# Optimization experiments

Measured on AMD Instinct MI355X. Metric: run time of the kernel, lower is better.

Reference implementation:

```python
import jax, jax.numpy as jnp
import numpy as np

N = 65536       # n_nodes
E = 1048576     # n_edges (avg degree 16)
D = 64          # in_features == out_features
GAMMA = 1.0


def setup_inputs() -> dict:
    key = jax.random.key(0)
    k_x, k_x0, k_ev, k_w, k_er, k_ec = jax.random.split(key, 6)
    x = jax.random.normal(k_x, (N, D), dtype=jnp.float32)
    x_0 = jax.random.normal(k_x0, (N, D), dtype=jnp.float32)
    edge_val = jax.random.uniform(k_ev, (E,), dtype=jnp.float32)
    # xavier_uniform for [D, D]: bound = sqrt(6 / (D + D))
    bound = np.sqrt(6.0 / (D + D)).astype(np.float32)
    weight = jax.random.uniform(k_w, (D, D), dtype=jnp.float32, minval=-bound, maxval=bound)
    bias = jnp.zeros((D,), dtype=jnp.float32)
    edge_row = jax.random.randint(k_er, (E,), 0, N, dtype=jnp.int32)
    edge_col = jax.random.randint(k_ec, (E,), 0, N, dtype=jnp.int32)
    return {"x": x, "x_0": x_0, "edge_val": edge_val, "weight": weight,
            "bias": bias, "edge_row": edge_row, "edge_col": edge_col}


def reference(x, x_0, edge_val, weight, bias, edge_row, edge_col):
    d = weight.shape[0]
    eye = jnp.eye(d, dtype=weight.dtype)
    s = weight - weight.T                      # skew-symmetric part
    m_left = eye - s
    m_right = eye + s
    # ortho_weight = solve(I + s, (I - s)^T)^T  (Cayley transform as written)
    ortho_weight = jnp.linalg.solve(m_right, m_left.T).T
    support = x @ ortho_weight                 # [N, D] dense GEMM
    # sparse adjacency spmm via COO gather + segment-sum
    gathered = edge_val[:, None] * support[edge_col]          # [E, D]
    agg = jax.ops.segment_sum(gathered, edge_row, num_segments=x.shape[0])  # [N, D]
    out = agg * GAMMA + x_0 + bias
    return out
```

## Files before the change

### kernel.cpp

```cpp
#include <hip/hip_runtime.h>
#include <math.h>


#define DFEAT 64
#define RPB   64
#define NPART_MAX 1024
#define EPB   4096
#define CURS  16
#define C_ROW 32
#define SPMM_T 512


__global__ void zero_ints_kernel(int* __restrict__ p, int n) {
    int i = blockIdx.x * blockDim.x + threadIdx.x;
    if (i < n) p[i] = 0;
}

__global__ void x_to_bf16_kernel(const float* __restrict__ x,
                                 unsigned short* __restrict__ x16, int n4) {
    int i = blockIdx.x * blockDim.x + threadIdx.x;
    if (i >= n4) return;
    float4 v = ((const float4*)x)[i];
    ushort4 o;
    unsigned u;
    u = __float_as_uint(v.x); o.x = (unsigned short)((u + 0x7FFFu + ((u >> 16) & 1u)) >> 16);
    u = __float_as_uint(v.y); o.y = (unsigned short)((u + 0x7FFFu + ((u >> 16) & 1u)) >> 16);
    u = __float_as_uint(v.z); o.z = (unsigned short)((u + 0x7FFFu + ((u >> 16) & 1u)) >> 16);
    u = __float_as_uint(v.w); o.w = (unsigned short)((u + 0x7FFFu + ((u >> 16) & 1u)) >> 16);
    ((ushort4*)x16)[i] = o;
}

__global__ __launch_bounds__(1024) void partition_build_kernel(
        const int* __restrict__ edge_row,
        const int* __restrict__ edge_col,
        const float* __restrict__ edge_val,
        int* __restrict__ scursor,
        int2* __restrict__ slists,
        int* __restrict__ ov_cursor,
        int2* __restrict__ ov_list,
        int E, int NP, int pcap) {
    __shared__ int cnt[NPART_MAX];
    __shared__ int off[NPART_MAX];
    int t = threadIdx.x;
    int base = blockIdx.x * EPB;
    int end = base + EPB; if (end > E) end = E;

    for (int i = t; i < NP; i += 1024) cnt[i] = 0;
    __syncthreads();
    for (int e = base + t; e < end; e += 1024)
        atomicAdd(&cnt[edge_row[e] >> 6], 1);
    __syncthreads();
    for (int p = t; p < NP; p += 1024) {
        int c = cnt[p];
        off[p] = (c > 0) ? atomicAdd(&scursor[p * CURS], c) : 0;
    }
    __syncthreads();
    for (int e = base + t; e < end; e += 1024) {
        int r = edge_row[e];
        int p = r >> 6;
        int2 ent;
        ent.x = (int)(((unsigned)r << 16) | (unsigned)edge_col[e]);
        ent.y = __float_as_int(edge_val[e]);
        int pos = atomicAdd(&off[p], 1);
        if (pos < pcap) {
            slists[(size_t)p * pcap + pos] = ent;
        } else {
            int op = atomicAdd(ov_cursor, 1);
            ov_list[op] = ent;
        }
    }
}

__global__ __launch_bounds__(SPMM_T) void spmm_fused_kernel(
        const unsigned short* __restrict__ x16,
        const float* __restrict__ x0,
        const float* __restrict__ bias,
        const int* __restrict__ scursor,
        const int2* __restrict__ slists,
        int* __restrict__ ov_cursor,
        int2* __restrict__ ov_list,
        float* __restrict__ out, int pcap) {
    __shared__ int2 bkt[RPB * C_ROW];
    __shared__ int  cur[RPB];
    int p = blockIdx.x;
    int t = threadIdx.x;

    if (t < RPB) cur[t] = 0;
    for (int i = t; i < RPB * C_ROW; i += SPMM_T) bkt[i] = make_int2(0, 0);
    __syncthreads();

    int cnt = scursor[p * CURS];
    if (cnt > pcap) cnt = pcap;
    const int2* list = slists + (size_t)p * pcap;
    for (int i = t; i < cnt; i += SPMM_T) {
        int2 ent = list[i];
        int row = (int)(((unsigned)ent.x >> 16) & (RPB - 1));
        int pos = atomicAdd(&cur[row], 1);
        if (pos < C_ROW) {
            bkt[row * C_ROW + pos] = ent;
        } else {
            int op = atomicAdd(ov_cursor, 1);
            ov_list[op] = ent;
        }
    }
    __syncthreads();

    int wave = t >> 6, lane = t & 63;
    float bl = bias[lane];
    for (int rr = wave; rr < RPB; rr += (SPMM_T / 64)) {
        int cr = cur[rr]; if (cr > C_ROW) cr = C_ROW;
        int cr8 = (cr + 7) & ~7;
        const int2* rb = &bkt[rr * C_ROW];
        float acc = 0.f;
        for (int j0 = 0; j0 < cr8; j0 += 8) {
            float xv[8], vv[8];
            #pragma unroll
            for (int k = 0; k < 8; k++) {
                int2 e = rb[j0 + k];
                vv[k] = __int_as_float(e.y);
                unsigned short hv =
                    x16[(size_t)((unsigned)e.x & 0xFFFFu) * DFEAT + lane];
                xv[k] = __uint_as_float((unsigned)hv << 16);
            }
            #pragma unroll
            for (int k = 0; k < 8; k++)
                acc += vv[k] * xv[k];
        }
        size_t go = (size_t)(p * RPB + rr) * DFEAT + lane;
        out[go] = acc + x0[go] + bl;
    }
}

__global__ void ov_drain_packed_kernel(const float* __restrict__ x,
                                       const int* __restrict__ ov_cursor,
                                       const int2* __restrict__ ov_list,
                                       float* __restrict__ out, int cap) {
    int n = ov_cursor[0];
    if (n > cap) n = cap;
    int wid = (blockIdx.x * blockDim.x + threadIdx.x) >> 6;
    int lane = threadIdx.x & 63;
    int nw = (gridDim.x * blockDim.x) >> 6;
    for (int k = wid; k < n; k += nw) {
        int2 p = ov_list[k];
        unsigned ux = (unsigned)p.x;
        int r = (int)(ux >> 16);
        int c = (int)(ux & 0xFFFFu);
        float v = __int_as_float(p.y);
        atomicAdd(&out[(size_t)r * DFEAT + lane],
                  v * x[(size_t)c * DFEAT + lane]);
    }
}


__global__ void bucket_scatter_kernel(const int* __restrict__ edge_row,
                                      const int* __restrict__ edge_col,
                                      const float* __restrict__ edge_val,
                                      int* __restrict__ cursor,
                                      int2* __restrict__ bucket,
                                      int* __restrict__ ov_cursor,
                                      int* __restrict__ ov_list,
                                      int E, int C) {
    int e = blockIdx.x * blockDim.x + threadIdx.x;
    if (e >= E) return;
    int r = edge_row[e];
    int pos = atomicAdd(&cursor[r], 1);
    if (pos < C) {
        int2 ent;
        ent.x = edge_col[e];
        ent.y = __float_as_int(edge_val[e]);
        bucket[(size_t)r * C + pos] = ent;
    } else {
        int op = atomicAdd(ov_cursor, 1);
        ov_list[op] = e;
    }
}

__global__ __launch_bounds__(256) void spmm_kernel(
        const float* __restrict__ x,
        const float* __restrict__ x0,
        const float* __restrict__ bias,
        const int* __restrict__ counts,
        const int2* __restrict__ bucket,
        float* __restrict__ out, int n, int C) {
    int wid = (blockIdx.x * blockDim.x + threadIdx.x) >> 6;
    int lane = threadIdx.x & 63;
    if (wid >= n) return;
    int cnt = counts[wid];
    if (cnt > C) cnt = C;
    const int2* bk = bucket + (size_t)wid * C;
    float acc = 0.f;
    for (int s0 = 0; s0 < cnt; s0 += 64) {
        int m = cnt - s0; if (m > 64) m = 64;
        int c = 0; float v = 0.f;
        if (lane < m) {
            int2 p = bk[s0 + lane];
            c = p.x;
            v = __int_as_float(p.y);
        }
        for (int j0 = 0; j0 < m; j0 += 8) {
            float xv[8], vv[8];
            #pragma unroll
            for (int k = 0; k < 8; k++) {
                int cj = __builtin_amdgcn_readlane(c, j0 + k);
                int vb = __builtin_amdgcn_readlane(__float_as_int(v), j0 + k);
                vv[k] = __int_as_float(vb);
                xv[k] = x[(size_t)cj * DFEAT + lane];
            }
            #pragma unroll
            for (int k = 0; k < 8; k++)
                acc += vv[k] * xv[k];
        }
    }
    out[(size_t)wid * DFEAT + lane] =
        acc + x0[(size_t)wid * DFEAT + lane] + bias[lane];
}

__global__ void ov_drain_id_kernel(const int* __restrict__ edge_row,
                                   const int* __restrict__ edge_col,
                                   const float* __restrict__ edge_val,
                                   const float* __restrict__ x,
                                   const int* __restrict__ ov_cursor,
                                   const int* __restrict__ ov_list,
                                   float* __restrict__ out, int E) {
    int n = ov_cursor[0];
    if (n > E) n = E;
    int wid = (blockIdx.x * blockDim.x + threadIdx.x) >> 6;
    int lane = threadIdx.x & 63;
    int nw = (gridDim.x * blockDim.x) >> 6;
    for (int k = wid; k < n; k += nw) {
        int e = ov_list[k];
        int r = edge_row[e], c = edge_col[e];
        float v = edge_val[e];
        atomicAdd(&out[(size_t)r * DFEAT + lane],
                  v * x[(size_t)c * DFEAT + lane]);
    }
}


__global__ void init_out_kernel(const float* __restrict__ x0,
                                const float* __restrict__ bias,
                                float* __restrict__ out, int n4) {
    int i = blockIdx.x * blockDim.x + threadIdx.x;
    if (i < n4) {
        float4 v = ((const float4*)x0)[i];
        int d = (i * 4) & (DFEAT - 1);
        v.x += bias[d + 0]; v.y += bias[d + 1];
        v.z += bias[d + 2]; v.w += bias[d + 3];
        ((float4*)out)[i] = v;
    }
}

__global__ void edge_scatter_kernel(const float* __restrict__ x,
                                    const float* __restrict__ edge_val,
                                    const int* __restrict__ edge_row,
                                    const int* __restrict__ edge_col,
                                    float* __restrict__ out, int E) {
    int tid = blockIdx.x * blockDim.x + threadIdx.x;
    int wave = tid >> 6, lane = tid & 63;
    int nwaves = (gridDim.x * blockDim.x) >> 6;
    for (int e = wave; e < E; e += nwaves) {
        int row = edge_row[e];
        int col = edge_col[e];
        float val = edge_val[e];
        atomicAdd(&out[row * DFEAT + lane], val * x[col * DFEAT + lane]);
    }
}

extern "C" void kernel_launch(void* const* d_in, const int* in_sizes, int n_in,
                              void* d_out, int out_size, void* d_ws, size_t ws_size,
                              hipStream_t stream) {
    const float* x    = (const float*)d_in[0];
    const float* x0   = (const float*)d_in[1];
    const float* ev   = (const float*)d_in[2];
    const float* bias = (const float*)d_in[4];
    const int*   er   = (const int*)d_in[5];
    const int*   ec   = (const int*)d_in[6];
    float* out = (float*)d_out;

    int E = in_sizes[2];
    int N = out_size / DFEAT;

    auto align256 = [](size_t b) { return (b + 255) & ~size_t(255); };

    if (N <= 65536 && N % RPB == 0 && E > 0) {
        int NP = N / RPB;
        double avg = (double)E / (double)NP;
        int pcap = (int)(avg + 6.0 * sqrt(avg > 1.0 ? avg : 1.0) + 64.0);

        size_t scur_b = align256((size_t)NP * CURS * 4);
        size_t ovc_b  = 256;
        size_t x16_b  = align256((size_t)N * DFEAT * 2);
        size_t ov_b   = align256((size_t)E * 8);
        size_t sl_b   = align256((size_t)NP * (size_t)pcap * 8);
        size_t total  = scur_b + ovc_b + x16_b + ov_b + sl_b;

        if (total <= ws_size) {
            char* ws = (char*)d_ws;
            int*            scursor = (int*)ws;
            int*            ovc     = (int*)(ws + scur_b);
            unsigned short* x16     = (unsigned short*)(ws + scur_b + ovc_b);
            int2*           ov_list = (int2*)(ws + scur_b + ovc_b + x16_b);
            int2*           slists  = (int2*)(ws + scur_b + ovc_b + x16_b + ov_b);

            int nzero = (int)((scur_b + ovc_b) / 4);
            zero_ints_kernel<<<(nzero + 255) / 256, 256, 0, stream>>>(scursor, nzero);
            int n4 = N * DFEAT / 4;
            x_to_bf16_kernel<<<(n4 + 255) / 256, 256, 0, stream>>>(x, x16, n4);
            int nblk = (E + EPB - 1) / EPB;
            partition_build_kernel<<<nblk, 1024, 0, stream>>>(
                er, ec, ev, scursor, slists, ovc, ov_list, E, NP, pcap);
            spmm_fused_kernel<<<NP, SPMM_T, 0, stream>>>(
                x16, x0, bias, scursor, slists, ovc, ov_list, out, pcap);
            ov_drain_packed_kernel<<<64, 256, 0, stream>>>(
                x, ovc, ov_list, out, E);
            return;
        }
    }

    {
        size_t cur_b = align256((size_t)N * 4);
        size_t ovc_b = 256;
        size_t ov_b  = align256((size_t)E * 4);
        size_t fixed = cur_b + ovc_b + ov_b;
        int C = 0;
        if (ws_size > fixed) {
            long long cmax = (long long)((ws_size - fixed) / ((size_t)N * 8));
            for (int cand : {64, 48, 40, 32, 28, 24})
                if (cmax >= cand) { C = cand; break; }
        }
        if (C >= 24) {
            char* ws = (char*)d_ws;
            int*  cursor  = (int*)ws;
            int*  ovc     = (int*)(ws + cur_b);
            int*  ov_list = (int*)(ws + cur_b + ovc_b);
            int2* bucket  = (int2*)(ws + fixed);

            int nzero = (int)((cur_b + ovc_b) / 4);
            zero_ints_kernel<<<(nzero + 255) / 256, 256, 0, stream>>>(cursor, nzero);
            bucket_scatter_kernel<<<(E + 255) / 256, 256, 0, stream>>>(
                er, ec, ev, cursor, bucket, ovc, ov_list, E, C);
            int blocks = (N * 64 + 255) / 256;
            spmm_kernel<<<blocks, 256, 0, stream>>>(
                x, x0, bias, cursor, bucket, out, N, C);
            ov_drain_id_kernel<<<64, 256, 0, stream>>>(
                er, ec, ev, x, ovc, ov_list, out, E);
            return;
        }
    }

    int n4 = out_size / 4;
    init_out_kernel<<<(n4 + 255) / 256, 256, 0, stream>>>(x0, bias, out, n4);
    edge_scatter_kernel<<<8192, 256, 0, stream>>>(x, ev, er, ec, out, E);
}
```

Baseline: 148.1 us.

## Replace global partition cursors with per-block private slot lists and fuse bf16 conversion

The partition build now gives each of 256 builder blocks a private fixed-capacity slot region per partition, so the global atomic cursor reservation and the per-block counting pass go away. Per-block counts are written to a table that the SpMM kernel reads to skip empty slots. The x-to-bf16 conversion is merged into the build kernel as extra blocks, which removes one launch and the large zeroing kernel. In exchange the SpMM kernel now scans 256×CAP slots per partition, many of them empty, and the sparse slot buffer is larger, which adds strided reads.

```diff
diff --git a/kernel.cpp b/kernel.cpp
--- a/kernel.cpp
+++ b/kernel.cpp
@@ -5,8 +5,7 @@
 #define DFEAT 64
 #define RPB   64
 #define NPART_MAX 1024
-#define EPB   4096
-#define CURS  16
+#define BBLK  256
 #define C_ROW 32
 #define SPMM_T 512
 
@@ -16,58 +15,62 @@
     if (i < n) p[i] = 0;
 }
 
-__global__ void x_to_bf16_kernel(const float* __restrict__ x,
-                                 unsigned short* __restrict__ x16, int n4) {
-    int i = blockIdx.x * blockDim.x + threadIdx.x;
-    if (i >= n4) return;
-    float4 v = ((const float4*)x)[i];
-    ushort4 o;
-    unsigned u;
-    u = __float_as_uint(v.x); o.x = (unsigned short)((u + 0x7FFFu + ((u >> 16) & 1u)) >> 16);
-    u = __float_as_uint(v.y); o.y = (unsigned short)((u + 0x7FFFu + ((u >> 16) & 1u)) >> 16);
-    u = __float_as_uint(v.z); o.z = (unsigned short)((u + 0x7FFFu + ((u >> 16) & 1u)) >> 16);
-    u = __float_as_uint(v.w); o.w = (unsigned short)((u + 0x7FFFu + ((u >> 16) & 1u)) >> 16);
-    ((ushort4*)x16)[i] = o;
-}
-
-__global__ __launch_bounds__(1024) void partition_build_kernel(
+__global__ __launch_bounds__(1024) void build_conv_kernel(
         const int* __restrict__ edge_row,
         const int* __restrict__ edge_col,
         const float* __restrict__ edge_val,
-        int* __restrict__ scursor,
+        const float* __restrict__ x,
+        unsigned short* __restrict__ x16,
+        int* __restrict__ cnt_blk,
         int2* __restrict__ slists,
         int* __restrict__ ov_cursor,
         int2* __restrict__ ov_list,
-        int E, int NP, int pcap) {
-    __shared__ int cnt[NPART_MAX];
-    __shared__ int off[NPART_MAX];
+        int E, int NP, int cap_shift, int n4) {
+    __shared__ int cur[NPART_MAX];
     int t = threadIdx.x;
-    int base = blockIdx.x * EPB;
-    int end = base + EPB; if (end > E) end = E;
-
-    for (int i = t; i < NP; i += 1024) cnt[i] = 0;
+
+    if (blockIdx.x >= BBLK) {
+        int i = (blockIdx.x - BBLK) * 1024 + t;
+        if (i < n4) {
+            float4 v = ((const float4*)x)[i];
+            ushort4 o;
+            unsigned u;
+            u = __float_as_uint(v.x); o.x = (unsigned short)((u + 0x7FFFu + ((u >> 16) & 1u)) >> 16);
+            u = __float_as_uint(v.y); o.y = (unsigned short)((u + 0x7FFFu + ((u >> 16) & 1u)) >> 16);
+            u = __float_as_uint(v.z); o.z = (unsigned short)((u + 0x7FFFu + ((u >> 16) & 1u)) >> 16);
+            u = __float_as_uint(v.w); o.w = (unsigned short)((u + 0x7FFFu + ((u >> 16) & 1u)) >> 16);
+            ((ushort4*)x16)[i] = o;
+        }
+        return;
+    }
+
+    int b = blockIdx.x;
+    int epb = (E + BBLK - 1) / BBLK;
+    int base = b * epb;
+    int end = base + epb; if (end > E) end = E;
+    int CAP = 1 << cap_shift;
+
+    for (int i = t; i < NP; i += 1024) cur[i] = 0;
     __syncthreads();
-    for (int e = base + t; e < end; e += 1024)
-        atomicAdd(&cnt[edge_row[e] >> 6], 1);
-    __syncthreads();
-    for (int p = t; p < NP; p += 1024) {
-        int c = cnt[p];
-        off[p] = (c > 0) ? atomicAdd(&scursor[p * CURS], c) : 0;
-    }
-    __syncthreads();
+
     for (int e = base + t; e < end; e += 1024) {
         int r = edge_row[e];
         int p = r >> 6;
         int2 ent;
         ent.x = (int)(((unsigned)r << 16) | (unsigned)edge_col[e]);
         ent.y = __float_as_int(edge_val[e]);
-        int pos = atomicAdd(&off[p], 1);
-        if (pos < pcap) {
-            slists[(size_t)p * pcap + pos] = ent;
+        int pos = atomicAdd(&cur[p], 1);
+        if (pos < CAP) {
+            slists[((((size_t)p << 8) | (size_t)b) << cap_shift) + pos] = ent;
         } else {
             int op = atomicAdd(ov_cursor, 1);
             ov_list[op] = ent;
         }
+    }
+    __syncthreads();
+    for (int p = t; p < NP; p += 1024) {
+        int c = cur[p];
+        cnt_blk[(size_t)b * NP + p] = (c > CAP) ? CAP : c;
     }
 }
 
@@ -75,32 +78,39 @@
         const unsigned short* __restrict__ x16,
         const float* __restrict__ x0,
         const float* __restrict__ bias,
-        const int* __restrict__ scursor,
+        const int* __restrict__ cnt_blk,
         const int2* __restrict__ slists,
         int* __restrict__ ov_cursor,
         int2* __restrict__ ov_list,
-        float* __restrict__ out, int pcap) {
+        float* __restrict__ out, int NP, int cap_shift) {
     __shared__ int2 bkt[RPB * C_ROW];
     __shared__ int  cur[RPB];
+    __shared__ int  ccnt[BBLK];
     int p = blockIdx.x;
     int t = threadIdx.x;
 
     if (t < RPB) cur[t] = 0;
+    for (int i = t; i < BBLK; i += SPMM_T)
+        ccnt[i] = cnt_blk[(size_t)i * NP + p];
     for (int i = t; i < RPB * C_ROW; i += SPMM_T) bkt[i] = make_int2(0, 0);
     __syncthreads();
 
-    int cnt = scursor[p * CURS];
-    if (cnt > pcap) cnt = pcap;
-    const int2* list = slists + (size_t)p * pcap;
-    for (int i = t; i < cnt; i += SPMM_T) {
-        int2 ent = list[i];
-        int row = (int)(((unsigned)ent.x >> 16) & (RPB - 1));
-        int pos = atomicAdd(&cur[row], 1);
-        if (pos < C_ROW) {
-            bkt[row * C_ROW + pos] = ent;
-        } else {
-            int op = atomicAdd(ov_cursor, 1);
-            ov_list[op] = ent;
+    int CAP = 1 << cap_shift;
+    int slots = BBLK << cap_shift;
+    const int2* list = slists + (((size_t)p << 8) << cap_shift);
+    for (int i = t; i < slots; i += SPMM_T) {
+        int b = i >> cap_shift;
+        int j = i & (CAP - 1);
+        if (j < ccnt[b]) {
+            int2 ent = list[i];
+            int row = (int)(((unsigned)ent.x >> 16) & (RPB - 1));
+            int pos = atomicAdd(&cur[row], 1);
+            if (pos < C_ROW) {
+                bkt[row * C_ROW + pos] = ent;
+            } else {
+                int op = atomicAdd(ov_cursor, 1);
+                ov_list[op] = ent;
+            }
         }
     }
     __syncthreads();
@@ -284,33 +294,35 @@
 
     if (N <= 65536 && N % RPB == 0 && E > 0) {
         int NP = N / RPB;
-        double avg = (double)E / (double)NP;
-        int pcap = (int)(avg + 6.0 * sqrt(avg > 1.0 ? avg : 1.0) + 64.0);
-
-        size_t scur_b = align256((size_t)NP * CURS * 4);
+        double lam = (double)E / ((double)NP * (double)BBLK);
+        double want = lam + 6.0 * sqrt(lam > 1.0 ? lam : 1.0);
+        int cap_shift = 4;
+        while ((double)(1 << cap_shift) < want && cap_shift < 10) cap_shift++;
+        size_t CAP = (size_t)1 << cap_shift;
+
         size_t ovc_b  = 256;
         size_t x16_b  = align256((size_t)N * DFEAT * 2);
         size_t ov_b   = align256((size_t)E * 8);
-        size_t sl_b   = align256((size_t)NP * (size_t)pcap * 8);
-        size_t total  = scur_b + ovc_b + x16_b + ov_b + sl_b;
+        size_t cnt_b  = align256((size_t)BBLK * (size_t)NP * 4);
+        size_t sl_b   = align256((size_t)NP * BBLK * CAP * 8);
+        size_t total  = ovc_b + x16_b + ov_b + cnt_b + sl_b;
 
         if (total <= ws_size) {
             char* ws = (char*)d_ws;
-            int*            scursor = (int*)ws;
-            int*            ovc     = (int*)(ws + scur_b);
-            unsigned short* x16     = (unsigned short*)(ws + scur_b + ovc_b);
-            int2*           ov_list = (int2*)(ws + scur_b + ovc_b + x16_b);
-            int2*           slists  = (int2*)(ws + scur_b + ovc_b + x16_b + ov_b);
-
-            int nzero = (int)((scur_b + ovc_b) / 4);
-            zero_ints_kernel<<<(nzero + 255) / 256, 256, 0, stream>>>(scursor, nzero);
+            int*            ovc     = (int*)ws;
+            unsigned short* x16     = (unsigned short*)(ws + ovc_b);
+            int2*           ov_list = (int2*)(ws + ovc_b + x16_b);
+            int*            cnt_blk = (int*)(ws + ovc_b + x16_b + ov_b);
+            int2*           slists  = (int2*)(ws + ovc_b + x16_b + ov_b + cnt_b);
+
+            zero_ints_kernel<<<1, 64, 0, stream>>>(ovc, 64);
             int n4 = N * DFEAT / 4;
-            x_to_bf16_kernel<<<(n4 + 255) / 256, 256, 0, stream>>>(x, x16, n4);
-            int nblk = (E + EPB - 1) / EPB;
-            partition_build_kernel<<<nblk, 1024, 0, stream>>>(
-                er, ec, ev, scursor, slists, ovc, ov_list, E, NP, pcap);
+            int conv_blocks = (n4 + 1023) / 1024;
+            build_conv_kernel<<<BBLK + conv_blocks, 1024, 0, stream>>>(
+                er, ec, ev, x, x16, cnt_blk, slists, ovc, ov_list,
+                E, NP, cap_shift, n4);
             spmm_fused_kernel<<<NP, SPMM_T, 0, stream>>>(
-                x16, x0, bias, scursor, slists, ovc, ov_list, out, pcap);
+                x16, x0, bias, cnt_blk, slists, ovc, ov_list, out, NP, cap_shift);
             ov_drain_packed_kernel<<<64, 256, 0, stream>>>(
                 x, ovc, ov_list, out, E);
             return;
```

After: 144.4 us. 1.03x faster.
